# Performance work log

Hardware: AMD Instinct MI355X
Metric: run time of the kernel (lower is better)

The kernel has to match this reference:

```python
import jax, jax.numpy as jnp
import numpy as np

K = 1.0            # curvature (manifold.k); sqrt(K)=1 simplifies formulas
EPS = 1e-5         # module eps used in variance rescale
MIN_NORM = 1e-8    # clamp for sqrt of Lorentz inners
MAX_EUCLID = 10.0  # rescale_to_max_euclid cap (keeps cosh/sinh in fp32 range)


def l_inner(x, y):
    # Lorentz inner product <x,y>_L = -x0*y0 + <x_s, y_s>, keepdim
    return -x[..., :1] * y[..., :1] + jnp.sum(x[..., 1:] * y[..., 1:], axis=-1, keepdims=True)


def centroid(x):
    # Lorentzian centroid over the group axis (dim=-2)
    avg = jnp.mean(x, axis=-2, keepdims=True)
    denom = jnp.sqrt(jnp.clip(-l_inner(avg, avg), MIN_NORM, None))
    return avg / denom


def logmap(x, y):
    alpha = jnp.clip(-l_inner(x, y), 1.0 + 1e-7, None)   # -<x,y>_L >= 1
    dist = jnp.arccosh(alpha)
    nomin = y - alpha * x                                # y + <x,y>_L * x
    denom = jnp.sqrt(jnp.clip(l_inner(nomin, nomin), MIN_NORM, None))
    return dist * nomin / denom


def _plus_origin(p):
    # p + o where o = (1, 0, ..., 0)
    return jnp.concatenate([p[..., :1] + 1.0, p[..., 1:]], axis=-1)


def transp0back(x, v):
    # parallel transport of tangent v at x back to the origin o
    nom = -v[..., :1]                 # <o, v>_L = -v0
    denom = 1.0 + x[..., :1]          # K - <x, o>_L = 1 + x0
    return v + (nom / denom) * _plus_origin(x)


def transp0(y, v):
    # parallel transport of tangent v at origin o to point y
    nom = l_inner(y, v)
    denom = 1.0 + y[..., :1]          # K - <o, y>_L = 1 + y0
    return v + (nom / denom) * _plus_origin(y)


def rescale_to_max_euclid(u):
    n = jnp.linalg.norm(u, axis=-1, keepdims=True)
    scale = jnp.minimum(1.0, MAX_EUCLID / jnp.clip(n, MIN_NORM, None))
    return u * scale


def expmap(x, u):
    nrm = jnp.sqrt(jnp.clip(l_inner(u, u), MIN_NORM, None))
    return jnp.cosh(nrm) * x + jnp.sinh(nrm) * (u / nrm)


def setup_inputs() -> dict:
    key = jax.random.key(0)
    k1, = jax.random.split(key, 1)
    bs, h, w, c = 64, 56, 56, 128
    # sample spatial components, lift onto the hyperboloid: x0 = sqrt(1+|xs|^2)
    xs = 0.5 * jax.random.normal(k1, (bs, h, w, c - 1), dtype=jnp.float32)
    x0 = jnp.sqrt(1.0 + jnp.sum(xs * xs, axis=-1, keepdims=True))
    x = jnp.concatenate([x0, xs], axis=-1)
    gamma = jnp.ones((c,), dtype=jnp.float32)
    # beta = manifold.origin(c) = (1, 0, ..., 0)
    beta = jnp.zeros((c,), dtype=jnp.float32).at[0].set(1.0)
    return {"x": x, "gamma": gamma, "beta": beta, "groups": 8}


def reference(x, gamma, beta, groups):
    bs, h, w, c = x.shape
    xg = x.reshape(bs, -1, groups, c)                    # (bs, hw/g, g, c)
    mean = centroid(xg)                                  # (bs, hw/g, 1, c)
    x_T = logmap(mean, xg)                               # tangent at mean
    x_T = transp0back(mean, x_T)                         # tangent at origin
    # Frechet-style variance: mean Euclidean norm over spatial dim (dim=1)
    var = jnp.mean(jnp.linalg.norm(x_T, axis=-1, keepdims=True), axis=1, keepdims=True)
    x_T = x_T * (gamma / (var + EPS))
    x_T = rescale_to_max_euclid(x_T)
    x_T = transp0(beta, x_T)                             # transport to beta
    out = expmap(beta, x_T)
    return out.reshape(bs, h, w, c)
```

## Files before the change

kernel.cpp:

```cpp
#include <hip/hip_runtime.h>
#include <math.h>


constexpr int S_GROUPS = 392;
constexpr int N_GROUPS = 64 * S_GROUPS;

__device__ __forceinline__ void wave_lds_fence() {
  __asm__ volatile("" ::: "memory");
  __builtin_amdgcn_wave_barrier();
  __asm__ volatile("" ::: "memory");
}

__device__ __forceinline__ void rsum8x3(float& a, float& b, float& c) {
#pragma unroll
  for (int m = 1; m <= 4; m <<= 1) {
    a += __shfl_xor(a, m, 64);
    b += __shfl_xor(b, m, 64);
    c += __shfl_xor(c, m, 64);
  }
}

__device__ __forceinline__ void fold_mean(const float v[16], int lane,
                                          float& c0, float& c1) {
  float a8[8];
  const bool h5 = (lane & 32) != 0;
#pragma unroll
  for (int i = 0; i < 8; ++i) {
    float kp = h5 ? v[i + 8] : v[i];
    float sd = h5 ? v[i] : v[i + 8];
    a8[i] = kp + __shfl_xor(sd, 32, 64);
  }
  float a4[4];
  const bool h4 = (lane & 16) != 0;
#pragma unroll
  for (int i = 0; i < 4; ++i) {
    float kp = h4 ? a8[i + 4] : a8[i];
    float sd = h4 ? a8[i] : a8[i + 4];
    a4[i] = kp + __shfl_xor(sd, 16, 64);
  }
  const bool h3 = (lane & 8) != 0;
  float kp0 = h3 ? a4[2] : a4[0], sd0 = h3 ? a4[0] : a4[2];
  float kp1 = h3 ? a4[3] : a4[1], sd1 = h3 ? a4[1] : a4[3];
  c0 = (kp0 + __shfl_xor(sd0, 8, 64)) * 0.125f;
  c1 = (kp1 + __shfl_xor(sd1, 8, 64)) * 0.125f;
}

struct CoreOut {
  float avg[16];
  float sc, k, coef;
  float iaL, dpL, yyE, y0p, avg0;
};

__device__ __forceinline__ void core(const float v[16], int lane,
                                     float* __restrict__ smrow, CoreOut& o) {
  const int p = lane >> 3, q = lane & 7;
  float c0, c1;
  fold_mean(v, lane, c0, c1);
  *reinterpret_cast<float2*>(&smrow[q * 16 + p * 2]) = make_float2(c0, c1);
  wave_lds_fence();
#pragma unroll
  for (int j = 0; j < 4; ++j)
    *reinterpret_cast<float4*>(&o.avg[4 * j]) =
        *reinterpret_cast<const float4*>(&smrow[q * 16 + 4 * j]);
  wave_lds_fence();

  float pa = 0.f, pd = 0.f, py = 0.f;
#pragma unroll
  for (int i = 0; i < 16; ++i) {
    pa = fmaf(o.avg[i], o.avg[i], pa);
    pd = fmaf(o.avg[i], v[i], pd);
    py = fmaf(v[i], v[i], py);
  }
  if (q == 0) {
    pa -= 2.f * o.avg[0] * o.avg[0];
    pd -= 2.f * o.avg[0] * v[0];
  }
  rsum8x3(pa, pd, py);
  o.iaL = pa;
  o.dpL = pd;
  o.yyE = py;
  o.y0p = __shfl(v[0], lane & 56, 64);
  o.avg0 = __shfl(o.avg[0], 0, 64);

  float rden = rsqrtf(fmaxf(-pa, 1e-8f));
  float a_raw = -pd * rden;
  float alpha = fmaxf(a_raw, 1.f + 1e-7f);
  float t = alpha - 1.f;
  float dist = log1pf(t + sqrtf(t * (alpha + 1.f)));
  float yyL = py - 2.f * o.y0p * o.y0p;
  float inn = fmaxf(yyL + 2.f * alpha * a_raw - alpha * alpha, 1e-8f);
  o.sc = dist * rsqrtf(inn);
  float am = alpha * rden;
  float mean0 = rden * o.avg0;
  float v0 = o.sc * (o.y0p - am * o.avg0);
  o.coef = -v0 / (1.f + mean0);
  o.k = o.coef * rden - o.sc * am;
}

__device__ __forceinline__ float xt_norm(const CoreOut& A) {
  float yavgE = A.dpL + 2.f * A.avg0 * A.y0p;
  float aaE = A.iaL + 2.f * A.avg0 * A.avg0;
  float nsq = A.sc * A.sc * A.yyE + A.k * A.k * aaE + 2.f * A.sc * A.k * yavgE +
              A.coef * A.coef + 2.f * A.coef * (A.sc * A.y0p + A.k * A.avg0);
  return sqrtf(fmaxf(nsq, 0.f));
}

__global__ __launch_bounds__(256) void lngn_pass1(const float* __restrict__ x,
                                                  float* __restrict__ var_part) {
  __shared__ float sm[4][2][128];
  const int w = threadIdx.x >> 6, lane = threadIdx.x & 63;
  const int p = lane >> 3, q = lane & 7;
  const int wid0 = (blockIdx.x * 4 + w) * 2;
  const float* b0 = x + (size_t)wid0 * 1024 + p * 128 + q * 16;
  float vA[16], vB[16];
#pragma unroll
  for (int j = 0; j < 4; ++j) {
    *reinterpret_cast<float4*>(&vA[4 * j]) =
        *reinterpret_cast<const float4*>(b0 + 4 * j);
    *reinterpret_cast<float4*>(&vB[4 * j]) =
        *reinterpret_cast<const float4*>(b0 + 1024 + 4 * j);
  }
  CoreOut A, B;
  core(vA, lane, sm[w][0], A);
  core(vB, lane, sm[w][1], B);
  float nA = xt_norm(A), nB = xt_norm(B);
  if (q == 0) {
    var_part[(size_t)wid0 * 8 + p] = nA;
    var_part[(size_t)(wid0 + 1) * 8 + p] = nB;
  }
}

__global__ __launch_bounds__(256) void lngn_finalize(
    const float* __restrict__ var_part, float* __restrict__ var_out) {
  const int wv = (int)((blockIdx.x * 256 + threadIdx.x) >> 6);
  const int lane = threadIdx.x & 63;
  const int b = wv >> 3, p = wv & 7;
  const float* base = var_part + (size_t)b * S_GROUPS * 8 + p;
  float s = 0.f;
  for (int s0 = lane; s0 < S_GROUPS; s0 += 64) s += base[(size_t)s0 * 8];
#pragma unroll
  for (int m = 32; m >= 1; m >>= 1) s += __shfl_xor(s, m, 64);
  if (lane == 0) var_out[wv] = s * (1.f / (float)S_GROUPS);
}

__global__ __launch_bounds__(256) void lngn_pass2(
    const float* __restrict__ x, const float* __restrict__ gamma,
    const float* __restrict__ beta, const float* __restrict__ var,
    float* __restrict__ out) {
  __shared__ float sm[4][128];
  const int w = threadIdx.x >> 6, lane = threadIdx.x & 63;
  const int p = lane >> 3, q = lane & 7;
  const int wid = blockIdx.x * 4 + w;
  const size_t base = (size_t)wid * 1024 + p * 128 + q * 16;
  float v[16];
#pragma unroll
  for (int j = 0; j < 4; ++j)
    *reinterpret_cast<float4*>(&v[4 * j]) =
        *reinterpret_cast<const float4*>(x + base + 4 * j);
  CoreOut C;
  core(v, lane, sm[w], C);

  const int b = wid / S_GROUPS;
  const float s1 = 1.f / (var[b * 8 + p] + 1e-5f);
  float gm[16], bt[16];
#pragma unroll
  for (int j = 0; j < 4; ++j) {
    *reinterpret_cast<float4*>(&gm[4 * j]) =
        *reinterpret_cast<const float4*>(gamma + q * 16 + 4 * j);
    *reinterpret_cast<float4*>(&bt[4 * j]) =
        *reinterpret_cast<const float4*>(beta + q * 16 + 4 * j);
  }

  float u[16];
  float pe = 0.f, pb = 0.f, pbb = 0.f;
#pragma unroll
  for (int i = 0; i < 16; ++i) {
    float xt = fmaf(C.sc, v[i], C.k * C.avg[i]);
    if (i == 0) xt += (q == 0) ? C.coef : 0.f;
    u[i] = xt * (gm[i] * s1);
    pe = fmaf(u[i], u[i], pe);
    pb = fmaf(bt[i], u[i], pb);
    pbb = fmaf(bt[i], bt[i], pbb);
  }
  if (q == 0) {
    pb -= 2.f * bt[0] * u[0];
    pbb -= 2.f * bt[0] * bt[0];
  }
  rsum8x3(pe, pb, pbb);
  const float u0 = __shfl(u[0], 0, 64);
  const float bt0 = __shfl(bt[0], 0, 64);

  float n = sqrtf(pe);
  float scl = fminf(1.f, 10.f / fmaxf(n, 1e-8f));
  float c2 = scl * pb / (1.f + bt0);
  float uuL = pe - 2.f * u0 * u0;
  float innw = scl * scl * uuL + 2.f * scl * c2 * (pb - u0) +
               c2 * c2 * (pbb - 2.f * bt0 - 1.f);
  float nrm = sqrtf(fmaxf(innw, 1e-8f));
  float e = expf(nrm), ie = 1.f / e;
  float chv = 0.5f * (e + ie);
  float isn = (0.5f * (e - ie)) / nrm;
  float C1 = chv + isn * c2, C2 = isn * scl, C3 = isn * c2;
  float o16[16];
#pragma unroll
  for (int i = 0; i < 16; ++i) o16[i] = fmaf(C1, bt[i], C2 * u[i]);
  if (q == 0) o16[0] += C3;
  float* ob = out + base;
#pragma unroll
  for (int j = 0; j < 4; ++j)
    *reinterpret_cast<float4*>(ob + 4 * j) =
        *reinterpret_cast<const float4*>(&o16[4 * j]);
}

extern "C" void kernel_launch(void* const* d_in, const int* in_sizes, int n_in,
                              void* d_out, int out_size, void* d_ws,
                              size_t ws_size, hipStream_t stream) {
  const float* x = (const float*)d_in[0];
  const float* gamma = (const float*)d_in[1];
  const float* beta = (const float*)d_in[2];
  float* out = (float*)d_out;
  float* var_part = (float*)d_ws;
  float* var_final = var_part + (size_t)N_GROUPS * 8;

  lngn_pass1<<<N_GROUPS / 8, 256, 0, stream>>>(x, var_part);
  lngn_finalize<<<128, 256, 0, stream>>>(var_part, var_final);
  lngn_pass2<<<N_GROUPS / 4, 256, 0, stream>>>(x, gamma, beta, var_final, out);
}
```

Measured before the change: 225.7 us.

## Cache per-group centroid and logmap coefficients from pass1 for reuse in pass2

Pass1 now writes each group's centroid (128 floats) and per-row scalars (sc, k, coef) to a workspace cache, and pass2 reads them back instead of redoing the centroid fold, LDS exchange and logmap scalar math. The var_part layout also changes to batch-major contiguous so the finalize reduction reads coalesced. This swaps recomputation in pass2 for extra global traffic, about 640 bytes per group written and read. Since the kernel is likely memory-bound, the added traffic could cost more than the compute it saves.

Result: slower. 232.5 us (+3.0%).

```diff
diff --git a/kernel.cpp b/kernel.cpp
--- a/kernel.cpp
+++ b/kernel.cpp
@@ -4,6 +4,7 @@
 
 constexpr int S_GROUPS = 392;
 constexpr int N_GROUPS = 64 * S_GROUPS;
+constexpr int CSTRIDE = 160;
 
 __device__ __forceinline__ void wave_lds_fence() {
   __asm__ volatile("" ::: "memory");
@@ -52,11 +53,13 @@
 };
 
 __device__ __forceinline__ void core(const float v[16], int lane,
-                                     float* __restrict__ smrow, CoreOut& o) {
+                                     float* __restrict__ smrow,
+                                     float* __restrict__ gc, CoreOut& o) {
   const int p = lane >> 3, q = lane & 7;
   float c0, c1;
   fold_mean(v, lane, c0, c1);
   *reinterpret_cast<float2*>(&smrow[q * 16 + p * 2]) = make_float2(c0, c1);
+  *reinterpret_cast<float2*>(&gc[q * 16 + p * 2]) = make_float2(c0, c1);
   wave_lds_fence();
 #pragma unroll
   for (int j = 0; j < 4; ++j)
@@ -95,6 +98,10 @@
   float v0 = o.sc * (o.y0p - am * o.avg0);
   o.coef = -v0 / (1.f + mean0);
   o.k = o.coef * rden - o.sc * am;
+
+  if (q == 0)
+    *reinterpret_cast<float4*>(&gc[128 + p * 4]) =
+        make_float4(o.sc, o.k, o.coef, 0.f);
 }
 
 __device__ __forceinline__ float xt_norm(const CoreOut& A) {
@@ -106,7 +113,8 @@
 }
 
 __global__ __launch_bounds__(256) void lngn_pass1(const float* __restrict__ x,
-                                                  float* __restrict__ var_part) {
+                                                  float* __restrict__ var_part,
+                                                  float* __restrict__ cache) {
   __shared__ float sm[4][2][128];
   const int w = threadIdx.x >> 6, lane = threadIdx.x & 63;
   const int p = lane >> 3, q = lane & 7;
@@ -121,12 +129,14 @@
         *reinterpret_cast<const float4*>(b0 + 1024 + 4 * j);
   }
   CoreOut A, B;
-  core(vA, lane, sm[w][0], A);
-  core(vB, lane, sm[w][1], B);
+  core(vA, lane, sm[w][0], cache + (size_t)wid0 * CSTRIDE, A);
+  core(vB, lane, sm[w][1], cache + (size_t)(wid0 + 1) * CSTRIDE, B);
   float nA = xt_norm(A), nB = xt_norm(B);
   if (q == 0) {
-    var_part[(size_t)wid0 * 8 + p] = nA;
-    var_part[(size_t)(wid0 + 1) * 8 + p] = nB;
+    const int b = wid0 / S_GROUPS;
+    const int s = wid0 - b * S_GROUPS;
+    var_part[(size_t)(b * 8 + p) * S_GROUPS + s] = nA;
+    var_part[(size_t)(b * 8 + p) * S_GROUPS + s + 1] = nB;
   }
 }
 
@@ -134,10 +144,9 @@
     const float* __restrict__ var_part, float* __restrict__ var_out) {
   const int wv = (int)((blockIdx.x * 256 + threadIdx.x) >> 6);
   const int lane = threadIdx.x & 63;
-  const int b = wv >> 3, p = wv & 7;
-  const float* base = var_part + (size_t)b * S_GROUPS * 8 + p;
+  const float* base = var_part + (size_t)wv * S_GROUPS;
   float s = 0.f;
-  for (int s0 = lane; s0 < S_GROUPS; s0 += 64) s += base[(size_t)s0 * 8];
+  for (int s0 = lane; s0 < S_GROUPS; s0 += 64) s += base[s0];
 #pragma unroll
   for (int m = 32; m >= 1; m >>= 1) s += __shfl_xor(s, m, 64);
   if (lane == 0) var_out[wv] = s * (1.f / (float)S_GROUPS);
@@ -146,37 +155,37 @@
 __global__ __launch_bounds__(256) void lngn_pass2(
     const float* __restrict__ x, const float* __restrict__ gamma,
     const float* __restrict__ beta, const float* __restrict__ var,
-    float* __restrict__ out) {
-  __shared__ float sm[4][128];
+    const float* __restrict__ cache, float* __restrict__ out) {
   const int w = threadIdx.x >> 6, lane = threadIdx.x & 63;
   const int p = lane >> 3, q = lane & 7;
   const int wid = blockIdx.x * 4 + w;
   const size_t base = (size_t)wid * 1024 + p * 128 + q * 16;
-  float v[16];
-#pragma unroll
-  for (int j = 0; j < 4; ++j)
+  const float* gc = cache + (size_t)wid * CSTRIDE;
+
+  float v[16], av[16], gm[16], bt[16];
+#pragma unroll
+  for (int j = 0; j < 4; ++j) {
     *reinterpret_cast<float4*>(&v[4 * j]) =
         *reinterpret_cast<const float4*>(x + base + 4 * j);
-  CoreOut C;
-  core(v, lane, sm[w], C);
-
-  const int b = wid / S_GROUPS;
-  const float s1 = 1.f / (var[b * 8 + p] + 1e-5f);
-  float gm[16], bt[16];
-#pragma unroll
-  for (int j = 0; j < 4; ++j) {
+    *reinterpret_cast<float4*>(&av[4 * j]) =
+        *reinterpret_cast<const float4*>(gc + q * 16 + 4 * j);
     *reinterpret_cast<float4*>(&gm[4 * j]) =
         *reinterpret_cast<const float4*>(gamma + q * 16 + 4 * j);
     *reinterpret_cast<float4*>(&bt[4 * j]) =
         *reinterpret_cast<const float4*>(beta + q * 16 + 4 * j);
   }
+  const float4 sk = *reinterpret_cast<const float4*>(gc + 128 + p * 4);
+  const float sc = sk.x, kk = sk.y, coef = sk.z;
+
+  const int b = wid / S_GROUPS;
+  const float s1 = 1.f / (var[b * 8 + p] + 1e-5f);
 
   float u[16];
   float pe = 0.f, pb = 0.f, pbb = 0.f;
 #pragma unroll
   for (int i = 0; i < 16; ++i) {
-    float xt = fmaf(C.sc, v[i], C.k * C.avg[i]);
-    if (i == 0) xt += (q == 0) ? C.coef : 0.f;
+    float xt = fmaf(sc, v[i], kk * av[i]);
+    if (i == 0) xt += (q == 0) ? coef : 0.f;
     u[i] = xt * (gm[i] * s1);
     pe = fmaf(u[i], u[i], pe);
     pb = fmaf(bt[i], u[i], pb);
@@ -221,8 +230,10 @@
   float* out = (float*)d_out;
   float* var_part = (float*)d_ws;
   float* var_final = var_part + (size_t)N_GROUPS * 8;
-
-  lngn_pass1<<<N_GROUPS / 8, 256, 0, stream>>>(x, var_part);
+  float* cache = var_final + 512;
+
+  lngn_pass1<<<N_GROUPS / 8, 256, 0, stream>>>(x, var_part, cache);
   lngn_finalize<<<128, 256, 0, stream>>>(var_part, var_final);
-  lngn_pass2<<<N_GROUPS / 4, 256, 0, stream>>>(x, gamma, beta, var_final, out);
-}
+  lngn_pass2<<<N_GROUPS / 4, 256, 0, stream>>>(x, gamma, beta, var_final, cache,
+                                               out);
+}
```
